# Kernel optimization log

Measured on AMD Instinct MI355X. Metric: run time of the kernel, lower is better.

Reference implementation:

```python
import jax, jax.numpy as jnp
import numpy as np

LAMBDA_CHAMFER = 1.0
LAMBDA_EDGE = 0.1


def setup_inputs() -> dict:
    key = jax.random.key(0)
    k1, k2, k3 = jax.random.split(key, 3)
    B, N, M, E = 8, 4096, 4096, 12288
    pred_vertices = jax.random.normal(k1, (B, N, 3), dtype=jnp.float32)
    gt_vertices = jax.random.normal(k2, (B, M, 3), dtype=jnp.float32)
    edges = jax.random.randint(k3, (E, 2), 0, N, dtype=jnp.int64)
    return {"pred_vertices": pred_vertices, "gt_vertices": gt_vertices, "edges": edges}


def _pairwise_dist(p1, p2):
    # ||x - y|| computed via the expanded form to avoid a [B,N,M,3] intermediate.
    # dist2[b,n,m] = |p1[b,n]|^2 + |p2[b,m]|^2 - 2 * p1[b,n] . p2[b,m]
    sq1 = jnp.sum(p1 * p1, axis=-1)  # [B, N]
    sq2 = jnp.sum(p2 * p2, axis=-1)  # [B, M]
    cross = jnp.einsum('bnd,bmd->bnm', p1, p2)  # [B, N, M]
    dist2 = sq1[:, :, None] + sq2[:, None, :] - 2.0 * cross
    return jnp.sqrt(jnp.maximum(dist2, 0.0))


def chamfer_distance(p1, p2):
    dist = _pairwise_dist(p1, p2)  # [B, N, M]
    min_p1 = jnp.min(dist, axis=2)  # [B, N] nearest gt for each pred point
    min_p2 = jnp.min(dist, axis=1)  # [B, M] nearest pred for each gt point
    return jnp.mean(min_p1) + jnp.mean(min_p2)


def edge_length_regularization(vertices, edges):
    v1 = vertices[:, edges[:, 0]]  # [B, E, 3]
    v2 = vertices[:, edges[:, 1]]  # [B, E, 3]
    lengths = jnp.linalg.norm(v1 - v2, axis=2)  # [B, E]
    return jnp.var(lengths, ddof=1)  # torch.var is unbiased by default


def reference(pred_vertices, gt_vertices, edges):
    cd = chamfer_distance(pred_vertices, gt_vertices)
    edge_loss = edge_length_regularization(pred_vertices, edges)
    return LAMBDA_CHAMFER * cd + LAMBDA_EDGE * edge_loss
```

## Files before the change

### kernel.cpp

```cpp
#include <hip/hip_runtime.h>
#include <hip/hip_bf16.h>
#include <float.h>

constexpr int B = 8, N = 4096, M = 4096, E = 12288;
constexpr int CBLOCK = 1024;
constexpr int EDGE_BLOCKS = (B * E) / CBLOCK;
constexpr int CHAM_BLOCKS = 2 * B * (N / 256);
constexpr int SPLIT = 32;
constexpr int RPT = M / SPLIT;
constexpr int VEC = 8;
constexpr int QB = 256;


__global__ __launch_bounds__(CBLOCK) void fused_kernel(
    const float* __restrict__ pred, const float* __restrict__ gt,
    const int* __restrict__ edges, float* __restrict__ ws) {
    const int bid = blockIdx.x;
    const int t = threadIdx.x;

    __shared__ float4 tile[M];
    __shared__ float wsum[16];
    float* red = (float*)tile;

    if (bid >= EDGE_BLOCKS) {
        const int cb  = bid - EDGE_BLOCKS;
        const int dir = cb >> 7;
        const int b   = (cb >> 4) & 7;
        const int qt  = cb & 15;
        const float* __restrict__ q   = dir ? gt   : pred;
        const float* __restrict__ ref = dir ? pred : gt;

        {
            const float2* rb = (const float2*)(ref + (size_t)b * M * 3) + 6 * t;
            const float2 r0 = rb[0], r1 = rb[1], r2 = rb[2];
            const float2 r3 = rb[3], r4 = rb[4], r5 = rb[5];
            const float x0=r0.x,y0=r0.y,z0=r1.x, x1=r1.y,y1=r2.x,z1=r2.y;
            const float x2=r3.x,y2=r3.y,z2=r4.x, x3=r4.y,y3=r5.x,z3=r5.y;
            tile[4*t+0] = make_float4(x0,y0,z0, 0.5f*(x0*x0+y0*y0+z0*z0));
            tile[4*t+1] = make_float4(x1,y1,z1, 0.5f*(x1*x1+y1*y1+z1*z1));
            tile[4*t+2] = make_float4(x2,y2,z2, 0.5f*(x2*x2+y2*y2+z2*z2));
            tile[4*t+3] = make_float4(x3,y3,z3, 0.5f*(x3*x3+y3*y3+z3*z3));
        }

        const int qloc = t & 31;
        const int s    = t >> 5;
        float qx[VEC], qy[VEC], qz[VEC], h1[VEC];
#pragma unroll
        for (int i = 0; i < VEC; i++) {
            const int n = qt * QB + qloc + i * 32;
            const float* qp = q + ((size_t)b * N + n) * 3;
            qx[i] = qp[0]; qy[i] = qp[1]; qz[i] = qp[2];
            h1[i] = 0.5f * (qx[i]*qx[i] + qy[i]*qy[i] + qz[i]*qz[i]);
        }
        __syncthreads();

        const float4* tl = tile + s * RPT;
        float mn[VEC];
#pragma unroll
        for (int i = 0; i < VEC; i++) mn[i] = FLT_MAX;

        float4 pA = tl[0], pB = tl[1];
#pragma unroll 2
        for (int m = 0; m < RPT - 2; m += 2) {
            const float4 nA = tl[m + 2], nB = tl[m + 3];
#pragma unroll
            for (int i = 0; i < VEC; i++) {
                float d0 = fmaf(-qx[i], pA.x, h1[i] + pA.w);
                d0 = fmaf(-qy[i], pA.y, d0);
                d0 = fmaf(-qz[i], pA.z, d0);
                float d1 = fmaf(-qx[i], pB.x, h1[i] + pB.w);
                d1 = fmaf(-qy[i], pB.y, d1);
                d1 = fmaf(-qz[i], pB.z, d1);
                mn[i] = fminf(mn[i], fminf(d0, d1));
            }
            pA = nA; pB = nB;
        }
#pragma unroll
        for (int i = 0; i < VEC; i++) {
            float d0 = fmaf(-qx[i], pA.x, h1[i] + pA.w);
            d0 = fmaf(-qy[i], pA.y, d0);
            d0 = fmaf(-qz[i], pA.z, d0);
            float d1 = fmaf(-qx[i], pB.x, h1[i] + pB.w);
            d1 = fmaf(-qy[i], pB.y, d1);
            d1 = fmaf(-qz[i], pB.z, d1);
            mn[i] = fminf(mn[i], fminf(d0, d1));
        }
        __syncthreads();

        const int wv = t >> 6;
#pragma unroll
        for (int i = 0; i < VEC; i++)
            mn[i] = fminf(mn[i], __shfl_xor(mn[i], 32, 64));
        if ((t & 32) == 0) {
#pragma unroll
            for (int i = 0; i < VEC; i++)
                red[(qloc + i * 32) + 256 * wv] = mn[i];
        }
        __syncthreads();

        float sv = 0.0f;
        if (t < QB) {
            float m = red[t];
#pragma unroll
            for (int w = 1; w < 16; w++) m = fminf(m, red[t + 256 * w]);
            sv = sqrtf(fmaxf(2.0f * m, 0.0f));
        }
#pragma unroll
        for (int o = 32; o > 0; o >>= 1) sv += __shfl_down(sv, o, 64);
        if ((t & 63) == 0) wsum[wv] = sv;
        __syncthreads();
        if (t == 0)
            ws[2 * EDGE_BLOCKS + cb] = wsum[0] + wsum[1] + wsum[2] + wsum[3];
    } else {
        const int eg = bid * CBLOCK + t;
        const int b  = eg / E;
        const int e  = eg - b * E;
        const int i0 = edges[2 * e], i1 = edges[2 * e + 1];
        const float* p0 = pred + ((size_t)b * N + i0) * 3;
        const float* p1 = pred + ((size_t)b * N + i1) * 3;
        const float dx = p0[0] - p1[0];
        const float dy = p0[1] - p1[1];
        const float dz = p0[2] - p1[2];
        float L  = sqrtf(dx * dx + dy * dy + dz * dz);
        float L2 = L * L;
#pragma unroll
        for (int o = 32; o > 0; o >>= 1) {
            L  += __shfl_down(L, o, 64);
            L2 += __shfl_down(L2, o, 64);
        }
        if ((t & 63) == 0) { red[t >> 6] = L; red[32 + (t >> 6)] = L2; }
        __syncthreads();
        if (t == 0) {
            float a = 0.0f, c = 0.0f;
#pragma unroll
            for (int w = 0; w < 16; w++) { a += red[w]; c += red[32 + w]; }
            ws[2 * bid]     = a;
            ws[2 * bid + 1] = c;
        }
    }
}

__global__ __launch_bounds__(256) void final_kernel(
    const float* __restrict__ ws, float* __restrict__ out) {
    const int t = threadIdx.x;
    float sc = ws[2 * EDGE_BLOCKS + t];
    float s1 = 0.0f, s2 = 0.0f;
    if (t < EDGE_BLOCKS) {
        s1 = ws[2 * t];
        s2 = ws[2 * t + 1];
    }
#pragma unroll
    for (int o = 32; o > 0; o >>= 1) {
        sc += __shfl_down(sc, o, 64);
        s1 += __shfl_down(s1, o, 64);
        s2 += __shfl_down(s2, o, 64);
    }
    __shared__ float w[3][4];
    const int wv = t >> 6, ln = t & 63;
    if (ln == 0) { w[0][wv] = sc; w[1][wv] = s1; w[2][wv] = s2; }
    __syncthreads();
    if (t == 0) {
        float S = 0.0f, A = 0.0f, C = 0.0f;
#pragma unroll
        for (int i = 0; i < 4; i++) { S += w[0][i]; A += w[1][i]; C += w[2][i]; }
        const float K = (float)(B * E);
        const float var = (C - A * A / K) / (K - 1.0f);
        out[0] = S / 32768.0f + 0.1f * var;
    }
}

extern "C" void kernel_launch(void* const* d_in, const int* in_sizes, int n_in,
                              void* d_out, int out_size, void* d_ws, size_t ws_size,
                              hipStream_t stream) {
    const float* pred  = (const float*)d_in[0];
    const float* gt    = (const float*)d_in[1];
    const int*   edges = (const int*)d_in[2];
    float* out = (float*)d_out;
    float* wsf = (float*)d_ws;

    fused_kernel<<<EDGE_BLOCKS + CHAM_BLOCKS, CBLOCK, 0, stream>>>(pred, gt, edges, wsf);
    final_kernel<<<1, 256, 0, stream>>>(wsf, out);
}
```

Baseline: 85.04 us.

## Hoist query norm out of inner loop and double per-thread query count

Measured after the change: 83.92 us. No clear change (-1.3%).

```diff
diff --git a/kernel.cpp b/kernel.cpp
--- a/kernel.cpp
+++ b/kernel.cpp
@@ -6,9 +6,9 @@
 constexpr int CBLOCK = 1024;
 constexpr int EDGE_BLOCKS = (B * E) / CBLOCK;
 constexpr int CHAM_BLOCKS = 2 * B * (N / 256);
-constexpr int SPLIT = 32;
+constexpr int SPLIT = 64;
 constexpr int RPT = M / SPLIT;
-constexpr int VEC = 8;
+constexpr int VEC = 16;
 constexpr int QB = 256;
 
 
@@ -42,15 +42,14 @@
             tile[4*t+3] = make_float4(x3,y3,z3, 0.5f*(x3*x3+y3*y3+z3*z3));
         }
 
-        const int qloc = t & 31;
-        const int s    = t >> 5;
-        float qx[VEC], qy[VEC], qz[VEC], h1[VEC];
+        const int qloc = t & 15;
+        const int s    = t >> 4;
+        float qx[VEC], qy[VEC], qz[VEC];
 #pragma unroll
         for (int i = 0; i < VEC; i++) {
-            const int n = qt * QB + qloc + i * 32;
+            const int n = qt * QB + qloc + i * 16;
             const float* qp = q + ((size_t)b * N + n) * 3;
             qx[i] = qp[0]; qy[i] = qp[1]; qz[i] = qp[2];
-            h1[i] = 0.5f * (qx[i]*qx[i] + qy[i]*qy[i] + qz[i]*qz[i]);
         }
         __syncthreads();
 
@@ -65,49 +64,45 @@
             const float4 nA = tl[m + 2], nB = tl[m + 3];
 #pragma unroll
             for (int i = 0; i < VEC; i++) {
-                float d0 = fmaf(-qx[i], pA.x, h1[i] + pA.w);
+                float d0 = fmaf(-qz[i], pA.z, pA.w);
                 d0 = fmaf(-qy[i], pA.y, d0);
-                d0 = fmaf(-qz[i], pA.z, d0);
-                float d1 = fmaf(-qx[i], pB.x, h1[i] + pB.w);
+                d0 = fmaf(-qx[i], pA.x, d0);
+                float d1 = fmaf(-qz[i], pB.z, pB.w);
                 d1 = fmaf(-qy[i], pB.y, d1);
-                d1 = fmaf(-qz[i], pB.z, d1);
+                d1 = fmaf(-qx[i], pB.x, d1);
                 mn[i] = fminf(mn[i], fminf(d0, d1));
             }
             pA = nA; pB = nB;
         }
 #pragma unroll
         for (int i = 0; i < VEC; i++) {
-            float d0 = fmaf(-qx[i], pA.x, h1[i] + pA.w);
+            float d0 = fmaf(-qz[i], pA.z, pA.w);
             d0 = fmaf(-qy[i], pA.y, d0);
-            d0 = fmaf(-qz[i], pA.z, d0);
-            float d1 = fmaf(-qx[i], pB.x, h1[i] + pB.w);
+            d0 = fmaf(-qx[i], pA.x, d0);
+            float d1 = fmaf(-qz[i], pB.z, pB.w);
             d1 = fmaf(-qy[i], pB.y, d1);
-            d1 = fmaf(-qz[i], pB.z, d1);
+            d1 = fmaf(-qx[i], pB.x, d1);
             mn[i] = fminf(mn[i], fminf(d0, d1));
         }
         __syncthreads();
 
-        const int wv = t >> 6;
 #pragma unroll
         for (int i = 0; i < VEC; i++)
-            mn[i] = fminf(mn[i], __shfl_xor(mn[i], 32, 64));
-        if ((t & 32) == 0) {
-#pragma unroll
-            for (int i = 0; i < VEC; i++)
-                red[(qloc + i * 32) + 256 * wv] = mn[i];
-        }
+            red[s * QB + qloc + i * 16] = mn[i];
         __syncthreads();
 
         float sv = 0.0f;
         if (t < QB) {
             float m = red[t];
-#pragma unroll
-            for (int w = 1; w < 16; w++) m = fminf(m, red[t + 256 * w]);
-            sv = sqrtf(fmaxf(2.0f * m, 0.0f));
+#pragma unroll 8
+            for (int k = 1; k < SPLIT; k++) m = fminf(m, red[k * QB + t]);
+            const float* qp = q + ((size_t)b * N + qt * QB + t) * 3;
+            const float sq = qp[0]*qp[0] + qp[1]*qp[1] + qp[2]*qp[2];
+            sv = sqrtf(fmaxf(2.0f * m + sq, 0.0f));
         }
 #pragma unroll
         for (int o = 32; o > 0; o >>= 1) sv += __shfl_down(sv, o, 64);
-        if ((t & 63) == 0) wsum[wv] = sv;
+        if ((t & 63) == 0) wsum[t >> 6] = sv;
         __syncthreads();
         if (t == 0)
             ws[2 * EDGE_BLOCKS + cb] = wsum[0] + wsum[1] + wsum[2] + wsum[3];
```
